# Optimization experiments

Measured on AMD Instinct MI355X. Metric: run time of the kernel, lower is better.

Reference implementation:

```python
import jax, jax.numpy as jnp
import numpy as np

EMBED = 256
HEADS = 8
HD = EMBED // HEADS
LEVELS = 4
POINTS = 4
FFN_H = 1024
BS = 8
LQ = 900
SHAPES = [(100, 100), (50, 50), (25, 25), (13, 13)]


def setup_inputs() -> dict:
    key = jax.random.key(0)
    ks = jax.random.split(key, 20)
    nv = sum(h * w for h, w in SHAPES)
    starts = np.cumsum([0] + [h * w for h, w in SHAPES])[:-1]
    inp = {
        "queries": jax.random.normal(ks[0], (BS, LQ, EMBED), jnp.float32),
        "memory": jax.random.normal(ks[1], (BS, nv, EMBED), jnp.float32),
        "query_pos": jax.random.normal(ks[2], (BS, LQ, EMBED), jnp.float32),
        "reference_points": jax.random.uniform(ks[3], (BS, LQ, LEVELS, 4), jnp.float32) * 0.9 + 0.05,
        "spatial_shapes": jnp.asarray(SHAPES, jnp.int32),
        "level_start_index": jnp.asarray(starts, jnp.int32),
    }
    def lin(k, din, dout):
        k1, k2 = jax.random.split(k)
        w = jax.random.normal(k1, (din, dout), jnp.float32) * 0.02
        b = jax.random.normal(k2, (dout,), jnp.float32) * 0.01
        return w, b
    specs = [("Wq", "bq", EMBED, EMBED), ("Wk", "bk", EMBED, EMBED), ("Wv", "bv", EMBED, EMBED),
             ("Wo", "bo", EMBED, EMBED), ("Wvd", "bvd", EMBED, EMBED),
             ("Woff", "boff", EMBED, HEADS * LEVELS * POINTS * 2),
             ("Watt", "batt", EMBED, HEADS * LEVELS * POINTS),
             ("Wop", "bop", EMBED, EMBED), ("Wg", "bg", 2 * EMBED, 2 * EMBED),
             ("W1", "b1", EMBED, FFN_H), ("W2", "b2", FFN_H, EMBED)]
    for i, (wn, bn, di, do) in enumerate(specs):
        w, b = lin(ks[4 + i], di, do)
        inp[wn] = w
        inp[bn] = b
    for n in ["ln1", "ln2", "ln3"]:
        inp[n + "_s"] = jnp.ones((EMBED,), jnp.float32)
        inp[n + "_b"] = jnp.zeros((EMBED,), jnp.float32)
    return inp


def _ln(x, s, b):
    m = jnp.mean(x, -1, keepdims=True)
    v = jnp.mean(jnp.square(x - m), -1, keepdims=True)
    return (x - m) * jax.lax.rsqrt(v + 1e-5) * s + b


def _bilinear(v_l, lx, ly, H, W):
    # v_l: [bs,h,H*W,hd]; lx,ly: [bs,h,lq,p] normalized in [0,1]
    # grid_sample(align_corners=False, padding=zeros) semantics
    px = lx * W - 0.5
    py = ly * H - 0.5
    x0 = jnp.floor(px)
    y0 = jnp.floor(py)
    wx = px - x0
    wy = py - y0
    x0i = x0.astype(jnp.int32)
    y0i = y0.astype(jnp.int32)
    bs, h, lq, p = lx.shape
    out = jnp.zeros((bs, h, lq, p, HD), v_l.dtype)
    for dy in (0, 1):
        for dx in (0, 1):
            xi = x0i + dx
            yi = y0i + dy
            w = (wx if dx else 1.0 - wx) * (wy if dy else 1.0 - wy)
            valid = (xi >= 0) & (xi < W) & (yi >= 0) & (yi < H)
            idx = jnp.clip(yi, 0, H - 1) * W + jnp.clip(xi, 0, W - 1)
            g = jnp.take_along_axis(v_l, idx.reshape(bs, h, lq * p)[..., None], axis=2)
            g = g.reshape(bs, h, lq, p, HD)
            out = out + w[..., None] * jnp.where(valid[..., None], g, 0.0)
    return out


def reference(queries, memory, query_pos, reference_points, spatial_shapes, level_start_index,
              Wq, bq, Wk, bk, Wv, bv, Wo, bo, Wvd, bvd, Woff, boff, Watt, batt, Wop, bop,
              Wg, bg, W1, b1, W2, b2, ln1_s, ln1_b, ln2_s, ln2_b, ln3_s, ln3_b):
    bs, lq, _ = queries.shape
    shp = np.asarray(spatial_shapes)
    st = np.asarray(level_start_index)

    # ---- self attention (pre-norm, q=k=x+pos, v=x) ----
    x = _ln(queries, ln1_s, ln1_b)
    qk = x + query_pos
    Q = (qk @ Wq + bq).reshape(bs, lq, HEADS, HD)
    K = (qk @ Wk + bk).reshape(bs, lq, HEADS, HD)
    V = (x @ Wv + bv).reshape(bs, lq, HEADS, HD)
    scores = jnp.einsum('bqhd,bkhd->bhqk', Q, K) * (1.0 / np.sqrt(HD))
    attn = jax.nn.softmax(scores, axis=-1)
    sa = jnp.einsum('bhqk,bkhd->bqhd', attn, V).reshape(bs, lq, EMBED) @ Wo + bo
    x1 = queries + sa  # dropout is identity in eval

    # ---- MS-deformable cross attention ----
    y = _ln(x1, ln2_s, ln2_b)
    qc = y + query_pos
    val = (memory @ Wvd + bvd).reshape(bs, -1, HEADS, HD).transpose(0, 2, 1, 3)  # [bs,h,Nv,hd]
    off = (qc @ Woff + boff).reshape(bs, lq, HEADS, LEVELS, POINTS, 2)
    aw = jax.nn.softmax((qc @ Watt + batt).reshape(bs, lq, HEADS, LEVELS * POINTS), axis=-1)
    aw = aw.reshape(bs, lq, HEADS, LEVELS, POINTS)
    rp = reference_points[:, :, None, :, None, :]  # [bs,lq,1,L,1,4]
    loc = rp[..., :2] + off / POINTS * rp[..., 2:] * 0.5  # [bs,lq,h,L,p,2]

    out = jnp.zeros((bs, HEADS, lq, HD), queries.dtype)
    for l in range(LEVELS):
        H, W = int(shp[l, 0]), int(shp[l, 1])
        s0 = int(st[l])
        v_l = val[:, :, s0:s0 + H * W]
        lx = jnp.transpose(loc[:, :, :, l, :, 0], (0, 2, 1, 3))  # [bs,h,lq,p]
        ly = jnp.transpose(loc[:, :, :, l, :, 1], (0, 2, 1, 3))
        samp = _bilinear(v_l, lx, ly, H, W)  # [bs,h,lq,p,hd]
        w = jnp.transpose(aw[:, :, :, l], (0, 2, 1, 3))  # [bs,h,lq,p]
        out = out + jnp.sum(w[..., None] * samp, axis=3)
    cross = out.transpose(0, 2, 1, 3).reshape(bs, lq, EMBED) @ Wop + bop

    # ---- gated fusion ----
    gi = jnp.concatenate([x1, cross], axis=-1)
    g = jax.nn.sigmoid(gi @ Wg + bg)
    x2 = g[..., :EMBED] * x1 + g[..., EMBED:] * cross

    # ---- FFN ----
    z = _ln(x2, ln3_s, ln3_b)
    ffn = jax.nn.relu(z @ W1 + b1) @ W2 + b2
    return (x2 + ffn, aw, loc)
```

## Files before the change

### kernel.cpp

```cpp
#include <hip/hip_runtime.h>
#include <hip/hip_bf16.h>
#include <math.h>

#define BB 8
#define LQ 900
#define EE 256
#define NH 8
#define HD 32
#define NL 4
#define NP 4
#define FFN_H 1024

typedef __bf16 bf16x8 __attribute__((ext_vector_type(8)));
typedef float f32x4 __attribute__((ext_vector_type(4)));
typedef unsigned short u16x8 __attribute__((ext_vector_type(8)));

__device__ __forceinline__ unsigned short f2b(float f) {
    union { float f; unsigned int u; } v; v.f = f;
    unsigned int u = v.u;
    unsigned int r = (u + 0x7fffu + ((u >> 16) & 1u)) >> 16;
    return (unsigned short)r;
}
__device__ __forceinline__ float b2f(unsigned short h) {
    union { unsigned int u; float f; } v; v.u = ((unsigned int)h) << 16; return v.f;
}

typedef __attribute__((address_space(3))) unsigned int* lds_ptr_t;
typedef const __attribute__((address_space(1))) unsigned int* gbl_ptr_t;
#define GLOAD16(g, l) __builtin_amdgcn_global_load_lds((gbl_ptr_t)(g), (lds_ptr_t)(l), 16, 0, 0)
#define VMCNT(n) asm volatile("s_waitcnt vmcnt(" #n ")" ::: "memory")
#define LGKM0()  asm volatile("s_waitcnt lgkmcnt(0)" ::: "memory")

struct TDesc { const float* src; unsigned short* dst; int K, N, tile0; };
struct TPack {
    TDesc d[11];
    const float *bq, *bk, *boff, *batt;
    float *bqk, *boa;
};

__global__ __launch_bounds__(256) void prep_kernel(
    TPack p,
    const float* __restrict__ queries, const float* __restrict__ qpos,
    const float* __restrict__ ln1_s, const float* __restrict__ ln1_b,
    unsigned short* __restrict__ x_b, unsigned short* __restrict__ qk_b)
{
    const int bi = blockIdx.x;
    const int t = threadIdx.x;

    if (bi < 1248) {
        int di = 0;
#pragma unroll
        for (int i = 1; i < 11; ++i) if (bi >= p.d[i].tile0) di = i;
        TDesc d = p.d[di];
        int tt = bi - d.tile0;
        int tn = (d.N + 31) >> 5;
        int tk = tt / tn, tc = tt % tn;
        __shared__ float tile[32][33];
        int tx = t & 31, ty = t >> 5;
#pragma unroll
        for (int i = 0; i < 4; ++i) {
            int kk = tk * 32 + ty + i * 8, nn = tc * 32 + tx;
            tile[ty + i * 8][tx] = d.src[(size_t)kk * d.N + nn];
        }
        __syncthreads();
#pragma unroll
        for (int i = 0; i < 4; ++i) {
            int nn = tc * 32 + ty + i * 8, kk = tk * 32 + tx;
            d.dst[(size_t)nn * d.K + kk] = f2b(tile[tx][ty + i * 8]);
        }
        return;
    }
    if (bi < 1252) {
        int which = bi - 1248;
        if (which == 0)      p.bqk[t] = p.bq[t];
        else if (which == 1) p.bqk[256 + t] = p.bk[t];
        else if (which == 2) p.boa[t] = p.boff[t];
        else if (t < 128)    p.boa[256 + t] = p.batt[t];
        return;
    }
    {
        const int row = bi - 1252;
        const int w = t >> 6, lane = t & 63;
        __shared__ float red[4];
        float v = queries[(size_t)row * EE + t];
        float sum = v;
#pragma unroll
        for (int o = 32; o; o >>= 1) sum += __shfl_xor(sum, o, 64);
        if (lane == 0) red[w] = sum;
        __syncthreads();
        float mean = (red[0] + red[1] + red[2] + red[3]) * (1.0f / 256.0f);
        __syncthreads();
        float dd = v - mean;
        float sq = dd * dd;
#pragma unroll
        for (int o = 32; o; o >>= 1) sq += __shfl_xor(sq, o, 64);
        if (lane == 0) red[w] = sq;
        __syncthreads();
        float var = (red[0] + red[1] + red[2] + red[3]) * (1.0f / 256.0f);
        float y = dd * rsqrtf(var + 1e-5f) * ln1_s[t] + ln1_b[t];
        x_b[(size_t)row * EE + t]  = f2b(y);
        qk_b[(size_t)row * EE + t] = f2b(y + qpos[(size_t)row * EE + t]);
    }
}

struct GD {
    const unsigned short* A;
    const float* Af;
    const unsigned short* Bt;
    const float* bias;
    const float* resid;
    float* outF;
    unsigned short* outB;
    const float* lnS; const float* lnB; const float* lnAdd;
    unsigned short* lnOut;
    int M, K, N, ntN, tile0, ldOutB, outBoff, act;
};
struct GB { GD d[3]; int nd, tot; };

template<int BN, bool AF32>
__global__ __launch_bounds__(256, (BN == 128) ? 4 : 2) void gemm_pipe(GB g) {
    __shared__ __align__(16) unsigned short ldsb[2][(64 + BN) * 32];
    __shared__ float lnred[2][64][2];
    const int tid = threadIdx.x;
    const int l = tid & 63, w = tid >> 6;
    const int wr = w >> 1, wc = w & 1;
    constexpr int NJ = BN / 32;

    int t = blockIdx.x;
    if (t >= g.tot) return;
    int d = 0;
    while (d + 1 < g.nd && t >= g.d[d + 1].tile0) ++d;

    const int sc = tid & 3;
    float4 fA[2];

    auto stage = [&](int dd, int tt, int ks, int pp) {
        const GD& D = g.d[dd];
        int local = tt - D.tile0;
        int m0 = (local / D.ntN) * 64;
        int n0 = (local % D.ntN) * BN;
        unsigned short* base = &ldsb[pp][0];
        if constexpr (AF32) {
            int row = tid >> 2;
            int rg = m0 + row; int mm = D.M - 1; rg = rg < mm ? rg : mm;
            int ck = (sc ^ ((row >> 1) & 3)) * 8;
            const float* src = D.Af + (size_t)rg * D.K + (ks << 5) + ck;
            fA[0] = *(const float4*)src;
            fA[1] = *(const float4*)(src + 4);
        } else {
            int row = w * 16 + (l >> 2);
            int rg = m0 + row; int mm = D.M - 1; rg = rg < mm ? rg : mm;
            int schunk = ((l & 3) ^ ((row >> 1) & 3)) << 4;
            GLOAD16((const char*)(D.A + (size_t)rg * D.K + (ks << 5)) + schunk,
                    base + (w * 16) * 32);
        }
#pragma unroll
        for (int ib = 0; ib < BN / 64; ++ib) {
            int row = ib * 64 + w * 16 + (l >> 2);
            int rg = n0 + row; int nn = D.N - 1; rg = rg < nn ? rg : nn;
            int schunk = ((l & 3) ^ ((row >> 1) & 3)) << 4;
            GLOAD16((const char*)(D.Bt + (size_t)rg * D.K + (ks << 5)) + schunk,
                    base + 2048 + (ib * 64 + w * 16) * 32);
        }
    };
    auto commitA = [&](int pp) {
        int row = tid >> 2;
        u16x8 o;
        o[0] = f2b(fA[0].x); o[1] = f2b(fA[0].y); o[2] = f2b(fA[0].z); o[3] = f2b(fA[0].w);
        o[4] = f2b(fA[1].x); o[5] = f2b(fA[1].y); o[6] = f2b(fA[1].z); o[7] = f2b(fA[1].w);
        *(u16x8*)((char*)&ldsb[pp][0] + row * 64 + sc * 16) = o;
    };

    stage(d, t, 0, 0);
    if constexpr (AF32) { commitA(0); LGKM0(); }
    int p = 0;

    while (true) {
        const GD D = g.d[d];
        int local = t - D.tile0;
        const int m0 = (local / D.ntN) * 64;
        const int n0 = (local % D.ntN) * BN;
        const int nk = D.K >> 5;

        f32x4 acc[2][NJ];
#pragma unroll
        for (int i = 0; i < 2; ++i)
#pragma unroll
            for (int j = 0; j < NJ; ++j) acc[i][j] = (f32x4){0.f, 0.f, 0.f, 0.f};

        for (int ks = 0; ks < nk; ++ks) {
            int nt = t, nks = ks + 1, ndd = d;
            bool have = true;
            if (nks == nk) {
                nt = t + gridDim.x; nks = 0;
                if (nt >= g.tot) have = false;
                else { while (ndd + 1 < g.nd && nt >= g.d[ndd + 1].tile0) ++ndd; }
            }
            if (have) {
                stage(ndd, nt, nks, p ^ 1);
                if constexpr (AF32)          { VMCNT(6); }
                else if constexpr (BN == 128){ VMCNT(3); }
                else                         { VMCNT(5); }
            } else {
                VMCNT(0);
            }
            __builtin_amdgcn_sched_barrier(0);
            __builtin_amdgcn_s_barrier();
            __builtin_amdgcn_sched_barrier(0);
            {
                const char* base = (const char*)&ldsb[p][0];
                const int rch = ((l >> 4) ^ ((l >> 1) & 3)) << 4;
                bf16x8 af[2];
#pragma unroll
                for (int i = 0; i < 2; ++i) {
                    int row = wr * 32 + i * 16 + (l & 15);
                    af[i] = *(const bf16x8*)(base + row * 64 + rch);
                }
#pragma unroll
                for (int j = 0; j < NJ; ++j) {
                    int row = wc * (BN / 2) + j * 16 + (l & 15);
                    bf16x8 bfr = *(const bf16x8*)(base + 4096 + row * 64 + rch);
#pragma unroll
                    for (int i = 0; i < 2; ++i)
                        acc[i][j] = __builtin_amdgcn_mfma_f32_16x16x32_bf16(af[i], bfr, acc[i][j], 0, 0, 0);
                }
            }
            if constexpr (AF32) {
                if (have) { commitA(p ^ 1); LGKM0(); }
            }
            __builtin_amdgcn_sched_barrier(0);
            __builtin_amdgcn_s_barrier();
            __builtin_amdgcn_sched_barrier(0);
            p ^= 1;
        }

#pragma unroll
        for (int i = 0; i < 2; ++i) {
#pragma unroll
            for (int r = 0; r < 4; ++r) {
                int gm = m0 + wr * 32 + i * 16 + ((l >> 4) << 2) + r;
                if (gm >= D.M) continue;
#pragma unroll
                for (int j = 0; j < NJ; ++j) {
                    int gn = n0 + wc * (BN / 2) + j * 16 + (l & 15);
                    if (gn >= D.N) continue;
                    float v = acc[i][j][r];
                    if (D.bias)  v += D.bias[gn];
                    if (D.resid) v += D.resid[(size_t)gm * D.N + gn];
                    if (D.act == 1)      v = fmaxf(v, 0.f);
                    else if (D.act == 2) v = 1.0f / (1.0f + __expf(-v));
                    acc[i][j][r] = v;
                    if (D.outF) D.outF[(size_t)gm * D.N + gn] = v;
                    if (D.outB) D.outB[(size_t)gm * D.ldOutB + D.outBoff + gn] = f2b(v);
                }
            }
        }

        if constexpr (BN == 256 && !AF32) {
            if (D.lnOut) {
#pragma unroll
                for (int i = 0; i < 2; ++i) {
#pragma unroll
                    for (int r = 0; r < 4; ++r) {
                        float s1 = 0.f, s2 = 0.f;
#pragma unroll
                        for (int j = 0; j < NJ; ++j) {
                            float v = acc[i][j][r];
                            s1 += v; s2 += v * v;
                        }
#pragma unroll
                        for (int o = 1; o <= 8; o <<= 1) {
                            s1 += __shfl_xor(s1, o, 64);
                            s2 += __shfl_xor(s2, o, 64);
                        }
                        if ((l & 15) == 0) {
                            int row = wr * 32 + i * 16 + ((l >> 4) << 2) + r;
                            lnred[wc][row][0] = s1;
                            lnred[wc][row][1] = s2;
                        }
                    }
                }
                __syncthreads();
#pragma unroll
                for (int i = 0; i < 2; ++i) {
#pragma unroll
                    for (int r = 0; r < 4; ++r) {
                        int row = wr * 32 + i * 16 + ((l >> 4) << 2) + r;
                        int gm = m0 + row;
                        if (gm >= D.M) continue;
                        float mean = (lnred[0][row][0] + lnred[1][row][0]) * (1.0f / 256.0f);
                        float msq  = (lnred[0][row][1] + lnred[1][row][1]) * (1.0f / 256.0f);
                        float rs = rsqrtf(msq - mean * mean + 1e-5f);
#pragma unroll
                        for (int j = 0; j < NJ; ++j) {
                            int gn = wc * (BN / 2) + j * 16 + (l & 15);
                            float y = (acc[i][j][r] - mean) * rs * D.lnS[gn] + D.lnB[gn]
                                      + D.lnAdd[(size_t)gm * 256 + gn];
                            D.lnOut[(size_t)gm * 256 + gn] = f2b(y);
                        }
                    }
                }
            }
        }

        t += gridDim.x;
        if (t >= g.tot) break;
        while (d + 1 < g.nd && t >= g.d[d + 1].tile0) ++d;
    }
}

__global__ __launch_bounds__(256) void attn_mfma(
    const unsigned short* __restrict__ QK, const unsigned short* __restrict__ Vb,
    unsigned short* __restrict__ outB)
{
    const int qt = blockIdx.x;
    const int bh = blockIdx.y;
    const int b = bh >> 3, h = bh & 7;
    const int tid = threadIdx.x;
    const int w = tid >> 6, l = tid & 63;

    __shared__ __align__(16) unsigned short Ks[64 * 32];
    __shared__ __align__(16) unsigned short VT[32 * 64];
    __shared__ __align__(16) unsigned short Ps[4][64 * 20];

    const int qrow_w = qt * 64 + w * 16;
    int qr = qrow_w + (l & 15); qr = qr < LQ ? qr : LQ - 1;
    bf16x8 qf = *(const bf16x8*)(QK + ((size_t)(b * LQ + qr)) * 512 + h * 32 + (l >> 4) * 8);

    f32x4 acc0 = {0.f, 0.f, 0.f, 0.f}, acc1 = {0.f, 0.f, 0.f, 0.f};
    float m_run = -1e30f, l_run = 0.f;
    const float scale = 0.17677669529663689f;
    const f32x4 z4 = {0.f, 0.f, 0.f, 0.f};

    const int key = tid >> 2;
    const int dg = (tid & 3) * 8;
    u16x8 kvc, vvc, kvn, vvn;
    {
        int krow = key; krow = krow < LQ ? krow : LQ - 1;
        size_t base = (size_t)(b * LQ + krow);
        kvc = *(const u16x8*)(QK + base * 512 + 256 + h * 32 + dg);
        vvc = *(const u16x8*)(Vb + base * 256 + h * 32 + dg);
    }

    for (int kt = 0; kt < 15; ++kt) {
        __syncthreads();
        *(u16x8*)((char*)Ks + key * 64 + ((dg * 2) ^ ((key & 3) << 4))) = kvc;
#pragma unroll
        for (int e = 0; e < 8; ++e) {
            int dd = dg + e;
            *(unsigned short*)((char*)VT + dd * 128 + ((key * 2) ^ ((dd & 7) << 4))) = vvc[e];
        }
        if (kt < 14) {
            int krow = (kt + 1) * 64 + key; krow = krow < LQ ? krow : LQ - 1;
            size_t base = (size_t)(b * LQ + krow);
            kvn = *(const u16x8*)(QK + base * 512 + 256 + h * 32 + dg);
            vvn = *(const u16x8*)(Vb + base * 256 + h * 32 + dg);
        }
        __syncthreads();

        float p[4][4];
        float tmax = -1e30f;
#pragma unroll
        for (int m = 0; m < 4; ++m) {
            int kr = m * 16 + (l & 15);
            bf16x8 kf = *(const bf16x8*)((const char*)Ks + kr * 64 +
                        (((l >> 4) * 16) ^ ((kr & 3) << 4)));
            f32x4 sf = __builtin_amdgcn_mfma_f32_16x16x32_bf16(kf, qf, z4, 0, 0, 0);
#pragma unroll
            for (int r = 0; r < 4; ++r) {
                int kk = kt * 64 + m * 16 + (l >> 4) * 4 + r;
                float sv = (kk < LQ) ? sf[r] * scale : -1e30f;
                p[m][r] = sv;
                tmax = fmaxf(tmax, sv);
            }
        }
        tmax = fmaxf(tmax, __shfl_xor(tmax, 16, 64));
        tmax = fmaxf(tmax, __shfl_xor(tmax, 32, 64));
        float newm = fmaxf(m_run, tmax);
        float corr = __expf(m_run - newm);
        m_run = newm;
        float tsum = 0.f;
#pragma unroll
        for (int m = 0; m < 4; ++m)
#pragma unroll
            for (int r = 0; r < 4; ++r) {
                float e = __expf(p[m][r] - newm);
                p[m][r] = e;
                tsum += e;
            }
        tsum += __shfl_xor(tsum, 16, 64);
        tsum += __shfl_xor(tsum, 32, 64);
        l_run = l_run * corr + tsum;
        acc0 *= corr;
        acc1 *= corr;

        unsigned short* pw = &Ps[w][0];
#pragma unroll
        for (int m = 0; m < 4; ++m)
#pragma unroll
            for (int r = 0; r < 4; ++r) {
                int kk = m * 16 + (l >> 4) * 4 + r;
                pw[kk * 20 + (l & 15)] = f2b(p[m][r]);
            }

#pragma unroll
        for (int s = 0; s < 2; ++s) {
            union { unsigned short u[8]; bf16x8 v; } pb;
#pragma unroll
            for (int j = 0; j < 8; ++j)
                pb.u[j] = pw[(s * 32 + (l >> 4) * 8 + j) * 20 + (l & 15)];
#pragma unroll
            for (int m2 = 0; m2 < 2; ++m2) {
                int dd = m2 * 16 + (l & 15);
                bf16x8 vf = *(const bf16x8*)((const char*)VT + dd * 128 +
                            ((s * 64 + (l >> 4) * 16) ^ ((dd & 7) << 4)));
                if (m2 == 0) acc0 = __builtin_amdgcn_mfma_f32_16x16x32_bf16(vf, pb.v, acc0, 0, 0, 0);
                else         acc1 = __builtin_amdgcn_mfma_f32_16x16x32_bf16(vf, pb.v, acc1, 0, 0, 0);
            }
        }
        if (kt < 14) { kvc = kvn; vvc = vvn; }
    }

    float inv = 1.0f / l_run;
    int q = qrow_w + (l & 15);
    if (q < LQ) {
        size_t obase = ((size_t)(b * LQ + q)) * 256 + h * 32;
#pragma unroll
        for (int r = 0; r < 4; ++r) {
            int d0 = (l >> 4) * 4 + r;
            outB[obase + d0]      = f2b(acc0[r] * inv);
            outB[obase + 16 + d0] = f2b(acc1[r] * inv);
        }
    }
}

__global__ __launch_bounds__(256) void sample_fused(
    const float* __restrict__ off_att, const float* __restrict__ refp,
    const unsigned short* __restrict__ val,
    const int* __restrict__ shapes, const int* __restrict__ starts,
    float* __restrict__ aw_out, float* __restrict__ loc_out,
    unsigned short* __restrict__ samp, int NV)
{
    const int row = blockIdx.x;
    const int b = row / LQ;
    const int t = threadIdx.x;
    const int h = t >> 5, d = t & 31;

    __shared__ float l_logit[128];
    __shared__ float l_aw[128];
    __shared__ float l_loc[256];
    __shared__ int l_sh[NL * 2];
    __shared__ int l_st[NL];

    if (t < 128) l_logit[t] = off_att[(size_t)row * 384 + 256 + t];
    {
        float o = off_att[(size_t)row * 384 + t];
        int c = t & 1;
        int lv = (t >> 3) & 3;
        float rc = refp[((size_t)row * 4 + lv) * 4 + c];
        float rs = refp[((size_t)row * 4 + lv) * 4 + 2 + c];
        float loc = rc + o * 0.125f * rs;
        l_loc[t] = loc;
        loc_out[(size_t)row * 256 + t] = loc;
    }
    if (t < NL * 2) l_sh[t] = shapes[t];
    if (t < NL) l_st[t] = starts[t];
    __syncthreads();
    if (t < 128) {
        int hh = t >> 4;
        float mx = -1e30f;
#pragma unroll
        for (int i = 0; i < 16; ++i) mx = fmaxf(mx, l_logit[hh * 16 + i]);
        float sum = 0.f;
#pragma unroll
        for (int i = 0; i < 16; ++i) sum += __expf(l_logit[hh * 16 + i] - mx);
        float aw = __expf(l_logit[t] - mx) / sum;
        l_aw[t] = aw;
        aw_out[(size_t)row * 128 + t] = aw;
    }
    __syncthreads();

    float acc = 0.f;
    const unsigned short* vb = val + (size_t)b * NV * EE + h * HD + d;

#pragma unroll
    for (int lv = 0; lv < NL; ++lv) {
        const int Hh = l_sh[lv * 2], Ww = l_sh[lv * 2 + 1];
        const int s0 = l_st[lv];
#pragma unroll
        for (int p = 0; p < NP; ++p) {
            const int base = ((h * NL + lv) * NP + p) * 2;
            float lx = l_loc[base], ly = l_loc[base + 1];
            float wgt0 = l_aw[h * 16 + lv * NP + p];
            float px = lx * (float)Ww - 0.5f;
            float py = ly * (float)Hh - 0.5f;
            float x0f = floorf(px), y0f = floorf(py);
            float wx = px - x0f, wy = py - y0f;
            int x0 = (int)x0f, y0 = (int)y0f;
#pragma unroll
            for (int dy = 0; dy < 2; ++dy) {
                int yi = y0 + dy;
                bool vy = (yi >= 0) && (yi < Hh);
                int yc = min(max(yi, 0), Hh - 1);
                float wyv = dy ? wy : 1.f - wy;
#pragma unroll
                for (int dx = 0; dx < 2; ++dx) {
                    int xi = x0 + dx;
                    bool vv = vy && (xi >= 0) && (xi < Ww);
                    int xc = min(max(xi, 0), Ww - 1);
                    float wgt = wgt0 * wyv * (dx ? wx : 1.f - wx);
                    float gv = b2f(vb[(size_t)(s0 + yc * Ww + xc) * EE]);
                    acc += vv ? wgt * gv : 0.f;
                }
            }
        }
    }
    samp[(size_t)row * EE + t] = f2b(acc);
}

__global__ __launch_bounds__(256) void gate_ln3(
    const float* __restrict__ g, const float* __restrict__ x1,
    const float* __restrict__ cross, const float* __restrict__ s,
    const float* __restrict__ bln, float* __restrict__ x2out,
    unsigned short* __restrict__ zb)
{
    const int row = blockIdx.x;
    const int t = threadIdx.x;
    const int w = t >> 6;
    const int lane = t & 63;
    __shared__ float red[4];

    float g1 = g[(size_t)row * 512 + t];
    float g2 = g[(size_t)row * 512 + 256 + t];
    float v = g1 * x1[(size_t)row * EE + t] + g2 * cross[(size_t)row * EE + t];
    x2out[(size_t)row * EE + t] = v;

    float sum = v;
#pragma unroll
    for (int o = 32; o; o >>= 1) sum += __shfl_xor(sum, o, 64);
    if (lane == 0) red[w] = sum;
    __syncthreads();
    float mean = (red[0] + red[1] + red[2] + red[3]) * (1.0f / 256.0f);
    __syncthreads();

    float d = v - mean;
    float sq = d * d;
#pragma unroll
    for (int o = 32; o; o >>= 1) sq += __shfl_xor(sq, o, 64);
    if (lane == 0) red[w] = sq;
    __syncthreads();
    float var = (red[0] + red[1] + red[2] + red[3]) * (1.0f / 256.0f);

    float y = d * rsqrtf(var + 1e-5f) * s[t] + bln[t];
    zb[(size_t)row * EE + t] = f2b(y);
}

extern "C" void kernel_launch(void* const* d_in, const int* in_sizes, int n_in,
                              void* d_out, int out_size, void* d_ws, size_t ws_size,
                              hipStream_t stream)
{
    const float* queries   = (const float*)d_in[0];
    const float* memory    = (const float*)d_in[1];
    const float* query_pos = (const float*)d_in[2];
    const float* refp      = (const float*)d_in[3];
    const int*   shapes    = (const int*)d_in[4];
    const int*   starts    = (const int*)d_in[5];
    const float* Wq  = (const float*)d_in[6],  *bq  = (const float*)d_in[7];
    const float* Wk  = (const float*)d_in[8],  *bk  = (const float*)d_in[9];
    const float* Wv  = (const float*)d_in[10], *bv  = (const float*)d_in[11];
    const float* Wo  = (const float*)d_in[12], *bo  = (const float*)d_in[13];
    const float* Wvd = (const float*)d_in[14], *bvd = (const float*)d_in[15];
    const float* Woff= (const float*)d_in[16], *boff= (const float*)d_in[17];
    const float* Watt= (const float*)d_in[18], *batt= (const float*)d_in[19];
    const float* Wop = (const float*)d_in[20], *bop = (const float*)d_in[21];
    const float* Wg  = (const float*)d_in[22], *bg  = (const float*)d_in[23];
    const float* W1  = (const float*)d_in[24], *b1  = (const float*)d_in[25];
    const float* W2  = (const float*)d_in[26], *b2  = (const float*)d_in[27];
    const float* ln1_s = (const float*)d_in[28], *ln1_b = (const float*)d_in[29];
    const float* ln2_s = (const float*)d_in[30], *ln2_b = (const float*)d_in[31];
    const float* ln3_s = (const float*)d_in[32], *ln3_b = (const float*)d_in[33];

    const int NV = in_sizes[1] / (BB * EE);
    const int Mq = BB * LQ;
    const int Mv = BB * NV;
    const long memN = (long)Mv * EE;

    char* W8 = (char*)d_ws;
    size_t off = 0;
    auto alloc = [&](size_t bytes) { char* p = W8 + off; off += (bytes + 255) & ~(size_t)255; return p; };

    unsigned short* val_b = (unsigned short*)alloc((size_t)memN * 2);
    unsigned short* WtQK  = (unsigned short*)alloc(512 * 256 * 2);
    unsigned short* WtV   = (unsigned short*)alloc(256 * 256 * 2);
    unsigned short* WtO   = (unsigned short*)alloc(256 * 256 * 2);
    unsigned short* WtVD  = (unsigned short*)alloc(256 * 256 * 2);
    unsigned short* WtOA  = (unsigned short*)alloc(384 * 256 * 2);
    unsigned short* WtOP  = (unsigned short*)alloc(256 * 256 * 2);
    unsigned short* WtG   = (unsigned short*)alloc(512 * 512 * 2);
    unsigned short* Wt1   = (unsigned short*)alloc(1024 * 256 * 2);
    unsigned short* Wt2   = (unsigned short*)alloc(256 * 1024 * 2);
    float*          bqk   = (float*)alloc(512 * 4);
    float*          boa   = (float*)alloc(384 * 4);
    unsigned short* qkb   = (unsigned short*)alloc((size_t)Mq * 512 * 2);
    unsigned short* vb_buf= (unsigned short*)alloc((size_t)Mq * 256 * 2);
    unsigned short* av_buf= (unsigned short*)alloc((size_t)Mq * 256 * 2);
    float*          x1    = (float*)alloc((size_t)Mq * 256 * 4);
    unsigned short* xc_cat= (unsigned short*)alloc((size_t)Mq * 512 * 2);
    unsigned short* qc_b  = (unsigned short*)alloc((size_t)Mq * 256 * 2);
    unsigned short* qk_b  = (unsigned short*)alloc((size_t)Mq * 256 * 2);
    float*          cross = (float*)alloc((size_t)Mq * 256 * 4);

    unsigned short* x_b = (unsigned short*)cross;
    float* off_att = (float*)qkb;
    unsigned short* samp_b = av_buf;
    float* gbuf = (float*)val_b;
    float* x2   = (float*)((char*)val_b + (size_t)Mq * 512 * 4);
    unsigned short* z_b = (unsigned short*)((char*)x2 + (size_t)Mq * 256 * 4);
    unsigned short* hidden_b = (unsigned short*)((char*)z_b + (size_t)Mq * 256 * 2);

    float* out0    = (float*)d_out;
    float* aw_out  = out0 + (size_t)Mq * 256;
    float* loc_out = aw_out + (size_t)Mq * 128;

    dim3 blk(256);
    const int tMq = (Mq + 63) / 64;
    const int tv  = (Mv + 63) / 64;

    TPack tp;
    tp.d[0]  = { Wq,   WtQK,             256, 256,    0 };
    tp.d[1]  = { Wk,   WtQK + 256 * 256, 256, 256,   64 };
    tp.d[2]  = { Wv,   WtV,              256, 256,  128 };
    tp.d[3]  = { Wo,   WtO,              256, 256,  192 };
    tp.d[4]  = { Wvd,  WtVD,             256, 256,  256 };
    tp.d[5]  = { Woff, WtOA,             256, 256,  320 };
    tp.d[6]  = { Watt, WtOA + 256 * 256, 256, 128,  384 };
    tp.d[7]  = { Wop,  WtOP,             256, 256,  416 };
    tp.d[8]  = { Wg,   WtG,              512, 512,  480 };
    tp.d[9]  = { W1,   Wt1,              256, 1024, 736 };
    tp.d[10] = { W2,   Wt2,             1024, 256,  992 };
    tp.bq = bq; tp.bk = bk; tp.boff = boff; tp.batt = batt;
    tp.bqk = bqk; tp.boa = boa;
    prep_kernel<<<1252 + Mq, blk, 0, stream>>>(
        tp, queries, query_pos, ln1_s, ln1_b, x_b, qk_b);

    {
        GB g; g.nd = 2;
        g.d[0] = { qk_b, nullptr, WtQK, bqk, nullptr, nullptr, qkb,
                   nullptr, nullptr, nullptr, nullptr,
                   Mq, 256, 512, 4, 0, 512, 0, 0 };
        g.d[1] = { x_b, nullptr, WtV, bv, nullptr, nullptr, vb_buf,
                   nullptr, nullptr, nullptr, nullptr,
                   Mq, 256, 256, 2, tMq * 4, 256, 0, 0 };
        g.tot = tMq * 6;
        gemm_pipe<128, false><<<g.tot, blk, 0, stream>>>(g);
    }

    {
        GB g; g.nd = 1;
        g.d[0] = { nullptr, memory, WtVD, bvd, nullptr, nullptr, val_b,
                   nullptr, nullptr, nullptr, nullptr,
                   Mv, 256, 256, 1, 0, 256, 0, 0 };
        g.tot = tv;
        gemm_pipe<256, true><<<831, blk, 0, stream>>>(g);
    }

    attn_mfma<<<dim3(15, BB * NH), blk, 0, stream>>>(qkb, vb_buf, av_buf);

    {
        GB g; g.nd = 1;
        g.d[0] = { av_buf, nullptr, WtO, bo, queries, x1, xc_cat,
                   ln2_s, ln2_b, query_pos, qc_b,
                   Mq, 256, 256, 1, 0, 512, 0, 0 };
        g.tot = tMq;
        gemm_pipe<256, false><<<tMq, blk, 0, stream>>>(g);
    }

    {
        GB g; g.nd = 1;
        g.d[0] = { qc_b, nullptr, WtOA, boa, nullptr, off_att, nullptr,
                   nullptr, nullptr, nullptr, nullptr,
                   Mq, 256, 384, 3, 0, 384, 0, 0 };
        g.tot = tMq * 3;
        gemm_pipe<128, false><<<g.tot, blk, 0, stream>>>(g);
    }

    sample_fused<<<Mq, blk, 0, stream>>>(off_att, refp, val_b, shapes, starts,
                                         aw_out, loc_out, samp_b, NV);

    {
        GB g; g.nd = 1;
        g.d[0] = { samp_b, nullptr, WtOP, bop, nullptr, cross, xc_cat,
                   nullptr, nullptr, nullptr, nullptr,
                   Mq, 256, 256, 2, 0, 512, 256, 0 };
        g.tot = tMq * 2;
        gemm_pipe<128, false><<<g.tot, blk, 0, stream>>>(g);
    }

    {
        GB g; g.nd = 1;
        g.d[0] = { xc_cat, nullptr, WtG, bg, nullptr, gbuf, nullptr,
                   nullptr, nullptr, nullptr, nullptr,
                   Mq, 512, 512, 4, 0, 512, 0, 2 };
        g.tot = tMq * 4;
        gemm_pipe<128, false><<<g.tot, blk, 0, stream>>>(g);
    }

    gate_ln3<<<Mq, blk, 0, stream>>>(gbuf, x1, cross, ln3_s, ln3_b, x2, z_b);

    {
        GB g; g.nd = 1;
        g.d[0] = { z_b, nullptr, Wt1, b1, nullptr, nullptr, hidden_b,
                   nullptr, nullptr, nullptr, nullptr,
                   Mq, 256, 1024, 8, 0, 1024, 0, 1 };
        g.tot = tMq * 8;
        gemm_pipe<128, false><<<g.tot, blk, 0, stream>>>(g);
    }

    {
        GB g; g.nd = 1;
        g.d[0] = { hidden_b, nullptr, Wt2, b2, x2, out0, nullptr,
                   nullptr, nullptr, nullptr, nullptr,
                   Mq, 1024, 256, 2, 0, 256, 0, 0 };
        g.tot = tMq * 2;
        gemm_pipe<128, false><<<g.tot, blk, 0, stream>>>(g);
    }
}
```

Before: 328.1 us.

## Merge memory value projection with QKV projections into one persistent GEMM launch

Turns the fp32-A path of the pipelined GEMM from a template parameter into a runtime per-descriptor flag. The memory value projection (fp32 input) and the QK/V projections (bf16 input) can then run in one grouped launch of 1536 persistent blocks using the 128-wide tile. This removes one kernel launch and the tail of each GEMM, and it rebalances tiles across CUs. In exchange, every GEMM pays runtime branches, and the value projection moves from 256-wide to 128-wide tiles, which may lower reuse.

```diff
diff --git a/kernel.cpp b/kernel.cpp
--- a/kernel.cpp
+++ b/kernel.cpp
@@ -113,11 +113,11 @@
     unsigned short* outB;
     const float* lnS; const float* lnB; const float* lnAdd;
     unsigned short* lnOut;
-    int M, K, N, ntN, tile0, ldOutB, outBoff, act;
+    int M, K, N, ntN, tile0, ldOutB, outBoff, act, aF32;
 };
 struct GB { GD d[3]; int nd, tot; };
 
-template<int BN, bool AF32>
+template<int BN>
 __global__ __launch_bounds__(256, (BN == 128) ? 4 : 2) void gemm_pipe(GB g) {
     __shared__ __align__(16) unsigned short ldsb[2][(64 + BN) * 32];
     __shared__ float lnred[2][64][2];
@@ -140,7 +140,7 @@
         int m0 = (local / D.ntN) * 64;
         int n0 = (local % D.ntN) * BN;
         unsigned short* base = &ldsb[pp][0];
-        if constexpr (AF32) {
+        if (D.aF32) {
             int row = tid >> 2;
             int rg = m0 + row; int mm = D.M - 1; rg = rg < mm ? rg : mm;
             int ck = (sc ^ ((row >> 1) & 3)) * 8;
@@ -172,7 +172,7 @@
     };
 
     stage(d, t, 0, 0);
-    if constexpr (AF32) { commitA(0); LGKM0(); }
+    if (g.d[d].aF32) { commitA(0); LGKM0(); }
     int p = 0;
 
     while (true) {
@@ -196,11 +196,14 @@
                 if (nt >= g.tot) have = false;
                 else { while (ndd + 1 < g.nd && nt >= g.d[ndd + 1].tile0) ++ndd; }
             }
+            bool stagedAF = have && g.d[ndd].aF32;
             if (have) {
                 stage(ndd, nt, nks, p ^ 1);
-                if constexpr (AF32)          { VMCNT(6); }
-                else if constexpr (BN == 128){ VMCNT(3); }
-                else                         { VMCNT(5); }
+                if (stagedAF) {
+                    if constexpr (BN == 128) { VMCNT(4); } else { VMCNT(6); }
+                } else {
+                    if constexpr (BN == 128) { VMCNT(3); } else { VMCNT(5); }
+                }
             } else {
                 VMCNT(0);
             }
@@ -225,9 +228,7 @@
                         acc[i][j] = __builtin_amdgcn_mfma_f32_16x16x32_bf16(af[i], bfr, acc[i][j], 0, 0, 0);
                 }
             }
-            if constexpr (AF32) {
-                if (have) { commitA(p ^ 1); LGKM0(); }
-            }
+            if (stagedAF) { commitA(p ^ 1); LGKM0(); }
             __builtin_amdgcn_sched_barrier(0);
             __builtin_amdgcn_s_barrier();
             __builtin_amdgcn_sched_barrier(0);
@@ -256,7 +257,7 @@
             }
         }
 
-        if constexpr (BN == 256 && !AF32) {
+        if constexpr (BN == 256) {
             if (D.lnOut) {
 #pragma unroll
                 for (int i = 0; i < 2; ++i) {
@@ -644,24 +645,18 @@
         tp, queries, query_pos, ln1_s, ln1_b, x_b, qk_b);
 
     {
-        GB g; g.nd = 2;
-        g.d[0] = { qk_b, nullptr, WtQK, bqk, nullptr, nullptr, qkb,
-                   nullptr, nullptr, nullptr, nullptr,
-                   Mq, 256, 512, 4, 0, 512, 0, 0 };
-        g.d[1] = { x_b, nullptr, WtV, bv, nullptr, nullptr, vb_buf,
-                   nullptr, nullptr, nullptr, nullptr,
-                   Mq, 256, 256, 2, tMq * 4, 256, 0, 0 };
-        g.tot = tMq * 6;
-        gemm_pipe<128, false><<<g.tot, blk, 0, stream>>>(g);
-    }
-
-    {
-        GB g; g.nd = 1;
+        GB g; g.nd = 3;
         g.d[0] = { nullptr, memory, WtVD, bvd, nullptr, nullptr, val_b,
                    nullptr, nullptr, nullptr, nullptr,
-                   Mv, 256, 256, 1, 0, 256, 0, 0 };
-        g.tot = tv;
-        gemm_pipe<256, true><<<831, blk, 0, stream>>>(g);
+                   Mv, 256, 256, 2, 0, 256, 0, 0, 1 };
+        g.d[1] = { qk_b, nullptr, WtQK, bqk, nullptr, nullptr, qkb,
+                   nullptr, nullptr, nullptr, nullptr,
+                   Mq, 256, 512, 4, tv * 2, 512, 0, 0, 0 };
+        g.d[2] = { x_b, nullptr, WtV, bv, nullptr, nullptr, vb_buf,
+                   nullptr, nullptr, nullptr, nullptr,
+                   Mq, 256, 256, 2, tv * 2 + tMq * 4, 256, 0, 0, 0 };
+        g.tot = tv * 2 + tMq * 6;
+        gemm_pipe<128><<<1536, blk, 0, stream>>>(g);
     }
 
     attn_mfma<<<dim3(15, BB * NH), blk, 0, stream>>>(qkb, vb_buf, av_buf);
@@ -670,18 +665,18 @@
         GB g; g.nd = 1;
         g.d[0] = { av_buf, nullptr, WtO, bo, queries, x1, xc_cat,
                    ln2_s, ln2_b, query_pos, qc_b,
-                   Mq, 256, 256, 1, 0, 512, 0, 0 };
+                   Mq, 256, 256, 1, 0, 512, 0, 0, 0 };
         g.tot = tMq;
-        gemm_pipe<256, false><<<tMq, blk, 0, stream>>>(g);
+        gemm_pipe<256><<<tMq, blk, 0, stream>>>(g);
     }
 
     {
         GB g; g.nd = 1;
         g.d[0] = { qc_b, nullptr, WtOA, boa, nullptr, off_att, nullptr,
                    nullptr, nullptr, nullptr, nullptr,
-                   Mq, 256, 384, 3, 0, 384, 0, 0 };
+                   Mq, 256, 384, 3, 0, 384, 0, 0, 0 };
         g.tot = tMq * 3;
-        gemm_pipe<128, false><<<g.tot, blk, 0, stream>>>(g);
+        gemm_pipe<128><<<g.tot, blk, 0, stream>>>(g);
     }
 
     sample_fused<<<Mq, blk, 0, stream>>>(off_att, refp, val_b, shapes, starts,
@@ -691,18 +686,18 @@
         GB g; g.nd = 1;
         g.d[0] = { samp_b, nullptr, WtOP, bop, nullptr, cross, xc_cat,
                    nullptr, nullptr, nullptr, nullptr,
-                   Mq, 256, 256, 2, 0, 512, 256, 0 };
+                   Mq, 256, 256, 2, 0, 512, 256, 0, 0 };
         g.tot = tMq * 2;
-        gemm_pipe<128, false><<<g.tot, blk, 0, stream>>>(g);
+        gemm_pipe<128><<<g.tot, blk, 0, stream>>>(g);
     }
 
     {
         GB g; g.nd = 1;
         g.d[0] = { xc_cat, nullptr, WtG, bg, nullptr, gbuf, nullptr,
                    nullptr, nullptr, nullptr, nullptr,
-                   Mq, 512, 512, 4, 0, 512, 0, 2 };
+                   Mq, 512, 512, 4, 0, 512, 0, 2, 0 };
         g.tot = tMq * 4;
-        gemm_pipe<128, false><<<g.tot, blk, 0, stream>>>(g);
+        gemm_pipe<128><<<g.tot, blk, 0, stream>>>(g);
     }
 
     gate_ln3<<<Mq, blk, 0, stream>>>(gbuf, x1, cross, ln3_s, ln3_b, x2, z_b);
@@ -711,17 +706,17 @@
         GB g; g.nd = 1;
         g.d[0] = { z_b, nullptr, Wt1, b1, nullptr, nullptr, hidden_b,
                    nullptr, nullptr, nullptr, nullptr,
-                   Mq, 256, 1024, 8, 0, 1024, 0, 1 };
+                   Mq, 256, 1024, 8, 0, 1024, 0, 1, 0 };
         g.tot = tMq * 8;
-        gemm_pipe<128, false><<<g.tot, blk, 0, stream>>>(g);
+        gemm_pipe<128><<<g.tot, blk, 0, stream>>>(g);
     }
 
     {
         GB g; g.nd = 1;
         g.d[0] = { hidden_b, nullptr, Wt2, b2, x2, out0, nullptr,
                    nullptr, nullptr, nullptr, nullptr,
-                   Mq, 1024, 256, 2, 0, 256, 0, 0 };
+                   Mq, 1024, 256, 2, 0, 256, 0, 0, 0 };
         g.tot = tMq * 2;
-        gemm_pipe<128, false><<<g.tot, blk, 0, stream>>>(g);
+        gemm_pipe<128><<<g.tot, blk, 0, stream>>>(g);
     }
 }
```

Measured after the change: 333.5 us. Within noise of the previous version (+1.6%).
